# Optimization experiments

Hardware: AMD Instinct MI355X
Metric: run time of the kernel (lower is better)

Reference implementation:

```python
import jax, jax.numpy as jnp
import numpy as np

# ---- layer config (yolov3, layer_no=2) ----
STRIDE = 8
N_CLASSES = 80
IGNORE_TH = 0.7
ANCHORS_PX = np.array([[10,13],[16,30],[33,23],[30,61],[62,45],[59,119],[116,90],[156,198],[373,326]], np.float32)
ALL_ANCHORS = ANCHORS_PX / STRIDE          # [9,2] in grid units
ANCHOR_ID_LO, ANCHOR_ID_HI = 0, 2          # anchor_mask[2] = [0,1,2]
ANCHORS = ALL_ANCHORS[ANCHOR_ID_LO:ANCHOR_ID_HI+1]  # [3,2]
NA = 3
NC = N_CLASSES + 5

B, IN_CH, NG, NBOX = 16, 256, 76, 50


def _safe_log(p):
    # emulate torch BCE's log clamp at -100; eps stops 0*inf -> nan
    return jnp.maximum(jnp.log(jnp.maximum(p, 1e-12)), -100.0)


def _bce_sum(p, t, w=None):
    l = -(t * _safe_log(p) + (1.0 - t) * _safe_log(1.0 - p))
    if w is not None:
        l = l * w
    return l.sum()


def setup_inputs() -> dict:
    key = jax.random.key(0)
    k1, k2, k3, k4, k5 = jax.random.split(key, 5)
    xin = jax.random.normal(k1, (B, IN_CH, NG, NG), jnp.float32)
    cls = jax.random.randint(k2, (B, NBOX, 1), 0, N_CLASSES).astype(jnp.float32)
    cxy = jax.random.uniform(k3, (B, NBOX, 2), jnp.float32, 0.02, 0.98)
    wh = jax.random.uniform(k4, (B, NBOX, 2), jnp.float32, 0.02, 0.40)
    labels = jnp.concatenate([cls, cxy, wh], axis=-1)  # [B,N,5]
    W = jax.random.normal(k5, (NA * NC, IN_CH), jnp.float32) * 0.02  # 1x1 conv
    b = jnp.zeros((NA * NC,), jnp.float32)
    return {"xin": xin, "labels": labels, "W": W, "b": b}


def _yolo_loss(xin, labels, W, b):
    nB, _, nG, _ = xin.shape
    anchors = jnp.asarray(ANCHORS, xin.dtype)          # [3,2]
    all_anchors = jnp.asarray(ALL_ANCHORS, xin.dtype)  # [9,2]

    # 1x1 conv -> [B, A, G, G, C]
    x = jnp.einsum('bchw,oc->bohw', xin, W) + b[None, :, None, None]
    x = x.reshape(nB, NA, NC, nG, nG).transpose(0, 1, 3, 4, 2)

    xy = jax.nn.sigmoid(x[..., :2])
    wh = x[..., 2:4]
    conf_cls = jax.nn.sigmoid(x[..., 4:])  # [B,A,G,G,1+ncls]

    gy, gx = jnp.meshgrid(jnp.arange(nG, dtype=x.dtype), jnp.arange(nG, dtype=x.dtype), indexing='ij')
    pred_boxes = jnp.stack([
        xy[..., 0] + gx,
        xy[..., 1] + gy,
        jnp.exp(wh[..., 0]) * anchors[:, 0][None, :, None, None],
        jnp.exp(wh[..., 1]) * anchors[:, 1][None, :, None, None]], axis=-1)  # [B,A,G,G,4]

    # ---- ground truth ----
    valid = labels.sum(-1) > 0                     # [B,N]
    gt_cls = labels[..., 0].astype(jnp.int32)
    gt = labels[..., 1:] * nG                      # [B,N,4] cx,cy,w,h in grid units
    gt_x, gt_y, gt_w, gt_h = gt[..., 0], gt[..., 1], gt[..., 2], gt[..., 3]
    gi = jnp.floor(gt_x).astype(jnp.int32)
    gj = jnp.floor(gt_y).astype(jnp.int32)

    # best anchor per gt: wh-IoU vs all 9 anchors (centered at origin)
    inter_a = jnp.minimum(gt_w[..., None], all_anchors[:, 0]) * jnp.minimum(gt_h[..., None], all_anchors[:, 1])
    union_a = gt_w[..., None] * gt_h[..., None] + all_anchors[:, 0] * all_anchors[:, 1] - inter_a
    best = jnp.argmax(inter_a / union_a, axis=-1)  # [B,N]
    in_mask = (best >= ANCHOR_ID_LO) & (best <= ANCHOR_ID_HI)
    a = jnp.where(in_mask, best % 3, -1)           # [B,N]

    # all-pairs IoU: pred boxes vs gt boxes (ignore mask)
    pb = pred_boxes.reshape(nB, -1, 4)             # [B,M,4], M = A*G*G
    pa_area = pb[..., 2] * pb[..., 3]
    gt_area = gt_w * gt_h
    tl = jnp.maximum(pb[:, :, None, :2] - pb[:, :, None, 2:] / 2, gt[:, None, :, :2] - gt[:, None, :, 2:] / 2)
    br = jnp.minimum(pb[:, :, None, :2] + pb[:, :, None, 2:] / 2, gt[:, None, :, :2] + gt[:, None, :, 2:] / 2)
    inter = jnp.prod(br - tl, -1) * jnp.all(tl < br, -1)
    iou = inter / (pa_area[:, :, None] + gt_area[:, None, :] - inter)
    iou = jnp.where(valid[:, None, :], iou, 0.0)
    best_iou = iou.max(-1)                         # [B,M]
    has_boxes = valid.any(-1)
    obj_mask = jnp.where(has_boxes[:, None], best_iou <= IGNORE_TH, True).reshape(nB, NA, nG, nG)

    # ---- scatter target assignment ----
    assign = valid & (a >= 0)
    a_safe = jnp.clip(a, 0, NA - 1)
    aw = anchors[a_safe, 0]
    ah = anchors[a_safe, 1]
    tvec = jnp.concatenate([
        (gt_x - jnp.floor(gt_x))[..., None],
        (gt_y - jnp.floor(gt_y))[..., None],
        jnp.log(gt_w / aw + 1e-16)[..., None],
        jnp.log(gt_h / ah + 1e-16)[..., None],
        jnp.ones_like(gt_x)[..., None],
        jax.nn.one_hot(gt_cls, N_CLASSES, dtype=x.dtype)], axis=-1)  # [B,N,NC]
    sval = 2.0 - gt_w * gt_h / (nG * nG)

    bf = jnp.broadcast_to(jnp.arange(nB)[:, None], a.shape).reshape(-1)
    af = jnp.where(assign, a_safe, NA).reshape(-1)  # NA is OOB -> dropped
    jf = gj.reshape(-1)
    if_ = gi.reshape(-1)

    target = jnp.zeros((nB, NA, nG, nG, NC), x.dtype).at[bf, af, jf, if_].set(tvec.reshape(-1, NC), mode='drop')
    scale = jnp.zeros((nB, NA, nG, nG), x.dtype).at[bf, af, jf, if_].set(sval.reshape(-1), mode='drop')
    obj_mask = obj_mask.at[bf, af, jf, if_].set(True, mode='drop')
    noobj = jnp.zeros((nB, NA, nG, nG), bool).at[bf, af, jf, if_].set(True, mode='drop')

    # ---- losses ----
    nm = noobj.astype(x.dtype)[..., None]
    p_obj = conf_cls[..., 0] * obj_mask
    t_obj = target[..., 4] * obj_mask
    p_xy = xy * nm
    t_xy = target[..., :2] * nm
    p_wh = wh * nm
    t_wh = target[..., 2:4] * nm
    p_cls = conf_cls[..., 1:] * nm
    t_cls = target[..., 5:] * nm
    sc = scale[..., None]

    loss_xy = _bce_sum(p_xy, t_xy, sc)
    rs = jnp.sqrt(sc)
    loss_wh = 0.5 * jnp.sum((p_wh * rs - t_wh * rs) ** 2)
    loss_obj = _bce_sum(p_obj, t_obj)
    loss_cls = _bce_sum(p_cls, t_cls)
    loss = loss_xy + loss_wh + loss_obj + loss_cls
    return jnp.stack([loss, loss_xy, loss_wh, loss_obj, loss_cls])


def reference(xin, labels, W, b):
    return _yolo_loss(xin, labels, W, b)
```

## Files before the change

kernel.cpp:

```cpp
#include <hip/hip_runtime.h>
#include <math.h>

#define NB    16
#define NAg   3
#define NCg   85
#define NCLS  80
#define NGg   76
#define NSp   (NGg*NGg)
#define NCELL (NAg*NSp)
#define NBOX  50
#define INCH  256

#define ACC_OFF  0
#define WIN_OFF  32
#define GD_OFF   (WIN_OFF + NB*NCELL*4)
#define GI_OFF   (GD_OFF + NB*NBOX*10*4)
#define PART_OFF (GI_OFF + NB*NBOX*2*4)
#define PART_SZ1 ((size_t)NB*15*NSp*4)
#define NEED4    (PART_OFF + 4*PART_SZ1)
#define NEED1    (PART_OFF + 1*PART_SZ1)
#define ZERO_BYTES GD_OFF

__device__ __constant__ float c_AW[9] = {1.25f,2.0f,4.125f,3.75f,7.75f,7.375f,14.5f,19.5f,46.625f};
__device__ __constant__ float c_AH[9] = {1.625f,3.75f,2.875f,7.625f,5.625f,14.875f,11.25f,24.75f,40.75f};

__device__ __forceinline__ float safe_log(float p) {
    return fmaxf(logf(fmaxf(p, 1e-12f)), -100.0f);
}
__device__ __forceinline__ float sigm(float x) {
    return 1.0f / (1.0f + expf(-x));
}

template<int NSLICE>
__global__ __launch_bounds__(256) void k_gemm_part(
    const float* __restrict__ xin, const float* __restrict__ W,
    float* __restrict__ part)
{
    constexpr int CPS = INCH / NSLICE;
    const int g  = blockIdx.x * 256 + threadIdx.x;
    if (g >= NSp/4) return;
    const int b  = blockIdx.y;
    const int sl = blockIdx.z;
    const int s0 = g * 4;

    float4 acc[15];
#pragma unroll
    for (int f = 0; f < 15; f++) acc[f] = make_float4(0.f,0.f,0.f,0.f);

    const float* xp = xin + ((size_t)b * INCH + sl * CPS) * NSp + s0;
    const float* wp = W + sl * CPS;
#pragma unroll 8
    for (int c = 0; c < CPS; c++) {
        const float4 v = *(const float4*)(xp + (size_t)c * NSp);
#pragma unroll
        for (int f = 0; f < 15; f++) {
            const int row = (f / 5) * NCg + (f % 5);
            const float w = wp[row * INCH + c];
            acc[f].x += w * v.x; acc[f].y += w * v.y;
            acc[f].z += w * v.z; acc[f].w += w * v.w;
        }
    }
#pragma unroll
    for (int f = 0; f < 15; f++)
        *(float4*)&part[(((size_t)sl * NB + b) * 15 + f) * NSp + s0] = acc[f];
}

__global__ void k_labels(const float* __restrict__ labels,
                         float* __restrict__ gdata, int* __restrict__ gint,
                         int* __restrict__ win)
{
    int t = blockIdx.x * blockDim.x + threadIdx.x;
    if (t >= NB * NBOX) return;
    int b = t / NBOX, n = t % NBOX;

    const float* L = labels + (size_t)t * 5;
    float l0 = L[0], l1 = L[1], l2 = L[2], l3 = L[3], l4 = L[4];
    int valid = (l0 + l1 + l2 + l3 + l4) > 0.f;

    float gx = l1 * NGg, gy = l2 * NGg, gw = l3 * NGg, gh = l4 * NGg;

    int best = 0; float brr = -1.f;
#pragma unroll
    for (int k = 0; k < 9; k++) {
        float inter = fminf(gw, c_AW[k]) * fminf(gh, c_AH[k]);
        float uni   = gw*gh + c_AW[k]*c_AH[k] - inter;
        float r     = inter / uni;
        if (r > brr) { brr = r; best = k; }
    }
    int a = (best <= 2) ? best : -1;
    int assign = valid && (a >= 0);
    int a_safe = a < 0 ? 0 : (a > 2 ? 2 : a);

    float* gd = gdata + (size_t)t * 10;
    gd[0] = gx; gd[1] = gy; gd[2] = gw; gd[3] = gh;
    gd[4] = gx - floorf(gx);
    gd[5] = gy - floorf(gy);
    gd[6] = logf(gw / c_AW[a_safe] + 1e-16f);
    gd[7] = logf(gh / c_AH[a_safe] + 1e-16f);
    gd[8] = 2.f - gw * gh / (float)NSp;
    gd[9] = valid ? 1.f : 0.f;

    int gi = (int)floorf(gx), gj = (int)floorf(gy);
    int inb = (gi >= 0) && (gi < NGg) && (gj >= 0) && (gj < NGg);
    int cell = (assign && inb) ? (a * NSp + gj * NGg + gi) : -1;
    gint[t*2 + 0] = cell;
    gint[t*2 + 1] = (int)l0;

    if (cell >= 0) atomicMax(&win[b * NCELL + cell], n + 1);
}

template<int NSLICE>
__global__ __launch_bounds__(256) void k_fuse(
    const float* __restrict__ part, const float* __restrict__ bias,
    const float* __restrict__ gdata, const int* __restrict__ win,
    float* __restrict__ acc)
{
    __shared__ float sb[NBOX][5];
    __shared__ int sHas;
    __shared__ float red[256];

    const int b = blockIdx.y;
    const int tid = threadIdx.x;

    if (tid < NBOX) {
        const float* gd = gdata + ((size_t)b * NBOX + tid) * 10;
        sb[tid][0] = gd[0]; sb[tid][1] = gd[1];
        sb[tid][2] = gd[2]; sb[tid][3] = gd[3];
        sb[tid][4] = gd[9];
    }
    if (tid == 0) sHas = 0;
    __syncthreads();
    if (tid < NBOX && sb[tid][4] > 0.f) atomicOr(&sHas, 1);
    __syncthreads();

    const int cell = blockIdx.x * 256 + tid;
    float l = 0.f;
    if (cell < NCELL) {
        const int a = cell / NSp, s = cell % NSp;
        float x0 = 0.f, x1 = 0.f, x2 = 0.f, x3 = 0.f, x4 = 0.f;
#pragma unroll
        for (int sl = 0; sl < NSLICE; sl++) {
            const float* pp = part + (((size_t)sl * NB + b) * 15 + a * 5) * NSp + s;
            x0 += pp[0*NSp]; x1 += pp[1*NSp]; x2 += pp[2*NSp];
            x3 += pp[3*NSp]; x4 += pp[4*NSp];
        }
        const float gxf = (float)(s % NGg);
        const float gyf = (float)(s / NGg);
        float px = sigm(x0 + bias[a*NCg+0]) + gxf;
        float py = sigm(x1 + bias[a*NCg+1]) + gyf;
        float pw = expf(x2 + bias[a*NCg+2]) * c_AW[a];
        float ph = expf(x3 + bias[a*NCg+3]) * c_AH[a];
        float cf = sigm(x4 + bias[a*NCg+4]);
        float pa = pw * ph;
        float bi = 0.f;
        for (int n = 0; n < NBOX; n++) {
            if (sb[n][4] > 0.f) {
                float gx = sb[n][0], gy = sb[n][1], gw = sb[n][2], gh = sb[n][3];
                float tlx = fmaxf(px - pw*0.5f, gx - gw*0.5f);
                float tly = fmaxf(py - ph*0.5f, gy - gh*0.5f);
                float brx = fminf(px + pw*0.5f, gx + gw*0.5f);
                float bry = fminf(py + ph*0.5f, gy + gh*0.5f);
                float inter = ((tlx < brx) && (tly < bry)) ? (brx-tlx)*(bry-tly) : 0.f;
                float iou = inter / (pa + gw*gh - inter);
                bi = fmaxf(bi, iou);
            }
        }
        bool maskpre  = sHas ? (bi <= 0.7f) : true;
        bool assigned = win[b * NCELL + cell] > 0;
        if (maskpre || assigned) {
            float t = assigned ? 1.f : 0.f;
            l = -(t * safe_log(cf) + (1.f - t) * safe_log(1.f - cf));
        }
    }
    red[tid] = l;
    __syncthreads();
    for (int o = 128; o > 0; o >>= 1) {
        if (tid < o) red[tid] += red[tid + o];
        __syncthreads();
    }
    if (tid == 0) atomicAdd(&acc[2], red[0]);
}

__global__ __launch_bounds__(256) void k_assigned(
    const float* __restrict__ xin, const float* __restrict__ W,
    const float* __restrict__ bias, const float* __restrict__ gdata,
    const int* __restrict__ gint, const int* __restrict__ win,
    float* __restrict__ acc)
{
    const int t = blockIdx.x;
    const int b = t / NBOX, n = t % NBOX;
    const int cell = gint[t*2];
    if (cell < 0) return;
    if (win[b * NCELL + cell] != n + 1) return;

    const int a = cell / NSp, s = cell % NSp;
    const int o0 = a * NCg;
    const int tid = threadIdx.x;

    __shared__ float4 col4[64];
    __shared__ float  xsh[NCg];
    __shared__ float  sacc[3];

    ((float*)col4)[tid] = xin[((size_t)b * INCH + tid) * NSp + s];
    if (tid < 3) sacc[tid] = 0.f;
    __syncthreads();

    const int wid = tid >> 6, lane = tid & 63;
    for (int o = wid; o < NCg; o += 4) {
        const float4 wv = *(const float4*)&W[(size_t)(o0 + o) * INCH + lane * 4];
        const float4 cv = col4[lane];
        float p = wv.x*cv.x + wv.y*cv.y + wv.z*cv.z + wv.w*cv.w;
        for (int off = 32; off; off >>= 1) p += __shfl_down(p, off);
        if (lane == 0) xsh[o] = p + bias[o0 + o];
    }
    __syncthreads();

    if (tid < NCg) {
        const float* gd = gdata + (size_t)t * 10;
        const float sval = gd[8];
        const int gcls = gint[t*2 + 1];
        float val = xsh[tid];
        float term; int slot;
        if (tid < 2) {
            float tgt = gd[4 + tid];
            float p = sigm(val);
            term = -(tgt * safe_log(p) + (1.f - tgt) * safe_log(1.f - p)) * sval;
            slot = 0;
        } else if (tid < 4) {
            float tgt = gd[4 + tid];
            float d = val - tgt;
            term = 0.5f * sval * d * d;
            slot = 1;
        } else if (tid == 4) {
            term = 0.f; slot = 2;
        } else {
            float tgt = ((tid - 5) == gcls) ? 1.f : 0.f;
            float p = sigm(val);
            term = -(tgt * safe_log(p) + (1.f - tgt) * safe_log(1.f - p));
            slot = 2;
        }
        atomicAdd(&sacc[slot], term);
    }
    __syncthreads();
    if (tid == 0) {
        atomicAdd(&acc[0], sacc[0]);
        atomicAdd(&acc[1], sacc[1]);
        atomicAdd(&acc[3], sacc[2]);
    }
}

__global__ void k_final(const float* __restrict__ acc, float* __restrict__ out)
{
    float xy = acc[0], wh = acc[1], ob = acc[2], cl = acc[3];
    out[0] = xy + wh + ob + cl;
    out[1] = xy; out[2] = wh; out[3] = ob; out[4] = cl;
}

extern "C" void kernel_launch(void* const* d_in, const int* in_sizes, int n_in,
                              void* d_out, int out_size, void* d_ws, size_t ws_size,
                              hipStream_t stream)
{
    const float* xin    = (const float*)d_in[0];
    const float* labels = (const float*)d_in[1];
    const float* W      = (const float*)d_in[2];
    const float* bias   = (const float*)d_in[3];

    char* ws = (char*)d_ws;
    float* acc   = (float*)(ws + ACC_OFF);
    int*   win   = (int*)  (ws + WIN_OFF);
    float* gdata = (float*)(ws + GD_OFF);
    int*   gint  = (int*)  (ws + GI_OFF);
    float* part  = (float*)(ws + PART_OFF);
    float* out   = (float*)d_out;

    const bool big = (ws_size >= (size_t)NEED4);

    hipMemsetAsync(ws, 0, ZERO_BYTES, stream);

    k_labels<<<dim3((NB*NBOX + 255)/256), 256, 0, stream>>>(labels, gdata, gint, win);

    const int gx = (NSp/4 + 255) / 256;
    if (big) k_gemm_part<4><<<dim3(gx, NB, 4), 256, 0, stream>>>(xin, W, part);
    else     k_gemm_part<1><<<dim3(gx, NB, 1), 256, 0, stream>>>(xin, W, part);

    const int fx = (NCELL + 255) / 256;
    if (big) k_fuse<4><<<dim3(fx, NB), 256, 0, stream>>>(part, bias, gdata, win, acc);
    else     k_fuse<1><<<dim3(fx, NB), 256, 0, stream>>>(part, bias, gdata, win, acc);

    k_assigned<<<dim3(NB*NBOX), 256, 0, stream>>>(xin, W, bias, gdata, gint, win, acc);
    k_final<<<1, 1, 0, stream>>>(acc, out);
}
```

Measured before the change: 203.1 us.

## Fuse partial GEMM and objectness loss into one kernel, drop winner map

Replaces the sliced partial-GEMM kernel plus the separate fuse kernel with a single kernel in which each thread computes all 15 needed conv outputs for one spatial position across the three anchors, then evaluates IoU and the objectness BCE in registers. A pre-transposed 16-wide weight table is built in the labels kernel. The per-cell winner array, with its large memset and atomics, is replaced by scanning the per-image box list for assignment and duplicate detection. The IoU threshold test is done by multiplication instead of division. This removes the partial-sum buffer round trip and the large zeroing, at the cost of a longer serial channel loop per thread with 64-thread blocks and lower parallelism.

```diff
diff --git a/kernel.cpp b/kernel.cpp
--- a/kernel.cpp
+++ b/kernel.cpp
@@ -7,19 +7,16 @@
 #define NCLS  80
 #define NGg   76
 #define NSp   (NGg*NGg)
-#define NCELL (NAg*NSp)
 #define NBOX  50
 #define INCH  256
 
 #define ACC_OFF  0
-#define WIN_OFF  32
-#define GD_OFF   (WIN_OFF + NB*NCELL*4)
-#define GI_OFF   (GD_OFF + NB*NBOX*10*4)
-#define PART_OFF (GI_OFF + NB*NBOX*2*4)
-#define PART_SZ1 ((size_t)NB*15*NSp*4)
-#define NEED4    (PART_OFF + 4*PART_SZ1)
-#define NEED1    (PART_OFF + 1*PART_SZ1)
-#define ZERO_BYTES GD_OFF
+#define HAS_OFF  32
+#define WT_OFF   128
+#define GB_OFF   (WT_OFF + 16384)
+#define GA_OFF   (GB_OFF + 25600)
+#define GI_OFF   (GA_OFF + 25600)
+#define ZERO_BYTES 96
 
 __device__ __constant__ float c_AW[9] = {1.25f,2.0f,4.125f,3.75f,7.75f,7.375f,14.5f,19.5f,46.625f};
 __device__ __constant__ float c_AH[9] = {1.625f,3.75f,2.875f,7.625f,5.625f,14.875f,11.25f,24.75f,40.75f};
@@ -31,53 +28,25 @@
     return 1.0f / (1.0f + expf(-x));
 }
 
-template<int NSLICE>
-__global__ __launch_bounds__(256) void k_gemm_part(
-    const float* __restrict__ xin, const float* __restrict__ W,
-    float* __restrict__ part)
-{
-    constexpr int CPS = INCH / NSLICE;
-    const int g  = blockIdx.x * 256 + threadIdx.x;
-    if (g >= NSp/4) return;
-    const int b  = blockIdx.y;
-    const int sl = blockIdx.z;
-    const int s0 = g * 4;
-
-    float4 acc[15];
-#pragma unroll
-    for (int f = 0; f < 15; f++) acc[f] = make_float4(0.f,0.f,0.f,0.f);
-
-    const float* xp = xin + ((size_t)b * INCH + sl * CPS) * NSp + s0;
-    const float* wp = W + sl * CPS;
-#pragma unroll 8
-    for (int c = 0; c < CPS; c++) {
-        const float4 v = *(const float4*)(xp + (size_t)c * NSp);
-#pragma unroll
-        for (int f = 0; f < 15; f++) {
-            const int row = (f / 5) * NCg + (f % 5);
-            const float w = wp[row * INCH + c];
-            acc[f].x += w * v.x; acc[f].y += w * v.y;
-            acc[f].z += w * v.z; acc[f].w += w * v.w;
-        }
-    }
-#pragma unroll
-    for (int f = 0; f < 15; f++)
-        *(float4*)&part[(((size_t)sl * NB + b) * 15 + f) * NSp + s0] = acc[f];
-}
-
-__global__ void k_labels(const float* __restrict__ labels,
-                         float* __restrict__ gdata, int* __restrict__ gint,
-                         int* __restrict__ win)
-{
-    int t = blockIdx.x * blockDim.x + threadIdx.x;
+__global__ __launch_bounds__(256) void k_labels(
+    const float* __restrict__ labels, const float* __restrict__ W,
+    float* __restrict__ Wt, float* __restrict__ gbox, float* __restrict__ gaux,
+    int* __restrict__ gint, int* __restrict__ hasAny)
+{
+    const int t = blockIdx.x * 256 + threadIdx.x;
+
+    if (t < INCH * 16) {
+        const int c = t >> 4, f = t & 15;
+        Wt[t] = (f < 15) ? W[((f / 5) * NCg + (f % 5)) * INCH + c] : 0.f;
+    }
     if (t >= NB * NBOX) return;
-    int b = t / NBOX, n = t % NBOX;
+    const int b = t / NBOX;
 
     const float* L = labels + (size_t)t * 5;
-    float l0 = L[0], l1 = L[1], l2 = L[2], l3 = L[3], l4 = L[4];
-    int valid = (l0 + l1 + l2 + l3 + l4) > 0.f;
-
-    float gx = l1 * NGg, gy = l2 * NGg, gw = l3 * NGg, gh = l4 * NGg;
+    const float l0 = L[0], l1 = L[1], l2 = L[2], l3 = L[3], l4 = L[4];
+    const int valid = (l0 + l1 + l2 + l3 + l4) > 0.f;
+
+    const float gx = l1 * NGg, gy = l2 * NGg, gw = l3 * NGg, gh = l4 * NGg;
 
     int best = 0; float brr = -1.f;
 #pragma unroll
@@ -87,111 +56,138 @@
         float r     = inter / uni;
         if (r > brr) { brr = r; best = k; }
     }
-    int a = (best <= 2) ? best : -1;
-    int assign = valid && (a >= 0);
-    int a_safe = a < 0 ? 0 : (a > 2 ? 2 : a);
-
-    float* gd = gdata + (size_t)t * 10;
-    gd[0] = gx; gd[1] = gy; gd[2] = gw; gd[3] = gh;
-    gd[4] = gx - floorf(gx);
-    gd[5] = gy - floorf(gy);
-    gd[6] = logf(gw / c_AW[a_safe] + 1e-16f);
-    gd[7] = logf(gh / c_AH[a_safe] + 1e-16f);
-    gd[8] = 2.f - gw * gh / (float)NSp;
-    gd[9] = valid ? 1.f : 0.f;
-
-    int gi = (int)floorf(gx), gj = (int)floorf(gy);
-    int inb = (gi >= 0) && (gi < NGg) && (gj >= 0) && (gj < NGg);
-    int cell = (assign && inb) ? (a * NSp + gj * NGg + gi) : -1;
+    const int a = (best <= 2) ? best : -1;
+    const int assign = valid && (a >= 0);
+    const int a_safe = a < 0 ? 0 : (a > 2 ? 2 : a);
+
+    const int gi = (int)floorf(gx), gj = (int)floorf(gy);
+    const int inb = (gi >= 0) && (gi < NGg) && (gj >= 0) && (gj < NGg);
+    const int cell = (assign && inb) ? (a * NSp + gj * NGg + gi) : -1;
+
+    float* gb = gbox + (size_t)t * 8;
+    gb[0] = gx - gw * 0.5f;
+    gb[1] = gy - gh * 0.5f;
+    gb[2] = gx + gw * 0.5f;
+    gb[3] = gy + gh * 0.5f;
+    gb[4] = valid ? gw * gh : -1.f;
+    gb[5] = __int_as_float(cell);
+
+    float* ga = gaux + (size_t)t * 8;
+    ga[0] = gx - floorf(gx);
+    ga[1] = gy - floorf(gy);
+    ga[2] = logf(gw / c_AW[a_safe] + 1e-16f);
+    ga[3] = logf(gh / c_AH[a_safe] + 1e-16f);
+    ga[4] = 2.f - gw * gh / (float)NSp;
+
     gint[t*2 + 0] = cell;
     gint[t*2 + 1] = (int)l0;
 
-    if (cell >= 0) atomicMax(&win[b * NCELL + cell], n + 1);
-}
-
-template<int NSLICE>
-__global__ __launch_bounds__(256) void k_fuse(
-    const float* __restrict__ part, const float* __restrict__ bias,
-    const float* __restrict__ gdata, const int* __restrict__ win,
-    float* __restrict__ acc)
-{
-    __shared__ float sb[NBOX][5];
-    __shared__ int sHas;
-    __shared__ float red[256];
-
+    if (valid) atomicOr(&hasAny[b], 1);
+}
+
+__global__ __launch_bounds__(64) void k_main(
+    const float* __restrict__ xin, const float* __restrict__ Wt,
+    const float* __restrict__ bias, const float* __restrict__ gbox,
+    const int* __restrict__ hasAny, float* __restrict__ acc)
+{
     const int b = blockIdx.y;
-    const int tid = threadIdx.x;
-
-    if (tid < NBOX) {
-        const float* gd = gdata + ((size_t)b * NBOX + tid) * 10;
-        sb[tid][0] = gd[0]; sb[tid][1] = gd[1];
-        sb[tid][2] = gd[2]; sb[tid][3] = gd[3];
-        sb[tid][4] = gd[9];
-    }
-    if (tid == 0) sHas = 0;
-    __syncthreads();
-    if (tid < NBOX && sb[tid][4] > 0.f) atomicOr(&sHas, 1);
-    __syncthreads();
-
-    const int cell = blockIdx.x * 256 + tid;
+    const int s = blockIdx.x * 64 + threadIdx.x;
+
     float l = 0.f;
-    if (cell < NCELL) {
-        const int a = cell / NSp, s = cell % NSp;
-        float x0 = 0.f, x1 = 0.f, x2 = 0.f, x3 = 0.f, x4 = 0.f;
-#pragma unroll
-        for (int sl = 0; sl < NSLICE; sl++) {
-            const float* pp = part + (((size_t)sl * NB + b) * 15 + a * 5) * NSp + s;
-            x0 += pp[0*NSp]; x1 += pp[1*NSp]; x2 += pp[2*NSp];
-            x3 += pp[3*NSp]; x4 += pp[4*NSp];
-        }
-        const float gxf = (float)(s % NGg);
-        const float gyf = (float)(s / NGg);
-        float px = sigm(x0 + bias[a*NCg+0]) + gxf;
-        float py = sigm(x1 + bias[a*NCg+1]) + gyf;
-        float pw = expf(x2 + bias[a*NCg+2]) * c_AW[a];
-        float ph = expf(x3 + bias[a*NCg+3]) * c_AH[a];
-        float cf = sigm(x4 + bias[a*NCg+4]);
-        float pa = pw * ph;
-        float bi = 0.f;
-        for (int n = 0; n < NBOX; n++) {
-            if (sb[n][4] > 0.f) {
-                float gx = sb[n][0], gy = sb[n][1], gw = sb[n][2], gh = sb[n][3];
-                float tlx = fmaxf(px - pw*0.5f, gx - gw*0.5f);
-                float tly = fmaxf(py - ph*0.5f, gy - gh*0.5f);
-                float brx = fminf(px + pw*0.5f, gx + gw*0.5f);
-                float bry = fminf(py + ph*0.5f, gy + gh*0.5f);
-                float inter = ((tlx < brx) && (tly < bry)) ? (brx-tlx)*(bry-tly) : 0.f;
-                float iou = inter / (pa + gw*gh - inter);
-                bi = fmaxf(bi, iou);
+    if (s < NSp) {
+        float accv[15];
+#pragma unroll
+        for (int f = 0; f < 15; ++f) accv[f] = 0.f;
+
+        const float* xp = xin + (size_t)b * INCH * NSp + s;
+#pragma unroll 2
+        for (int c0 = 0; c0 < INCH; c0 += 8) {
+            float v[8];
+#pragma unroll
+            for (int k = 0; k < 8; ++k) v[k] = xp[(size_t)(c0 + k) * NSp];
+#pragma unroll
+            for (int k = 0; k < 8; ++k) {
+                const float* wr = Wt + ((c0 + k) << 4);
+#pragma unroll
+                for (int f = 0; f < 15; ++f) accv[f] += wr[f] * v[k];
             }
         }
-        bool maskpre  = sHas ? (bi <= 0.7f) : true;
-        bool assigned = win[b * NCELL + cell] > 0;
-        if (maskpre || assigned) {
-            float t = assigned ? 1.f : 0.f;
-            l = -(t * safe_log(cf) + (1.f - t) * safe_log(1.f - cf));
-        }
-    }
-    red[tid] = l;
-    __syncthreads();
-    for (int o = 128; o > 0; o >>= 1) {
-        if (tid < o) red[tid] += red[tid + o];
-        __syncthreads();
-    }
-    if (tid == 0) atomicAdd(&acc[2], red[0]);
+
+        const int sy = s / NGg;
+        const int sx = s - sy * NGg;
+        const float gxf = (float)sx, gyf = (float)sy;
+
+        float pbx0[3], pby0[3], pbx1[3], pby1[3], pa[3], cf[3];
+#pragma unroll
+        for (int a = 0; a < 3; ++a) {
+            const float px = sigm(accv[a*5+0] + bias[a*NCg+0]) + gxf;
+            const float py = sigm(accv[a*5+1] + bias[a*NCg+1]) + gyf;
+            const float pw = expf(accv[a*5+2] + bias[a*NCg+2]) * c_AW[a];
+            const float ph = expf(accv[a*5+3] + bias[a*NCg+3]) * c_AH[a];
+            cf[a]  = sigm(accv[a*5+4] + bias[a*NCg+4]);
+            pbx0[a] = px - pw * 0.5f;  pby0[a] = py - ph * 0.5f;
+            pbx1[a] = px + pw * 0.5f;  pby1[a] = py + ph * 0.5f;
+            pa[a]   = pw * ph;
+        }
+
+        bool ex0 = false, ex1 = false, ex2 = false;
+        bool as0 = false, as1 = false, as2 = false;
+        const float* gb = gbox + (size_t)b * NBOX * 8;
+        for (int n = 0; n < NBOX; ++n) {
+            const float bx0 = gb[n*8+0], by0 = gb[n*8+1];
+            const float bx1 = gb[n*8+2], by1 = gb[n*8+3];
+            const float gar = gb[n*8+4];
+            const int cell  = __float_as_int(gb[n*8+5]);
+            const int d = cell - s;
+            as0 = as0 || (d == 0);
+            as1 = as1 || (d == NSp);
+            as2 = as2 || (d == 2*NSp);
+            if (gar >= 0.f) {
+#pragma unroll
+                for (int a = 0; a < 3; ++a) {
+                    const float tlx = fmaxf(pbx0[a], bx0);
+                    const float tly = fmaxf(pby0[a], by0);
+                    const float brx = fminf(pbx1[a], bx1);
+                    const float bry = fminf(pby1[a], by1);
+                    const float dx = brx - tlx, dy = bry - tly;
+                    const float inter = (dx > 0.f && dy > 0.f) ? dx * dy : 0.f;
+                    const bool hit = inter > 0.7f * (pa[a] + gar - inter);
+                    if      (a == 0) ex0 = ex0 || hit;
+                    else if (a == 1) ex1 = ex1 || hit;
+                    else             ex2 = ex2 || hit;
+                }
+            }
+        }
+
+        const bool hasB = hasAny[b] != 0;
+#pragma unroll
+        for (int a = 0; a < 3; ++a) {
+            const bool ex = (a == 0) ? ex0 : ((a == 1) ? ex1 : ex2);
+            const bool as = (a == 0) ? as0 : ((a == 1) ? as1 : as2);
+            const bool maskpre = hasB ? (!ex) : true;
+            if (maskpre || as) {
+                const float c = cf[a];
+                l += as ? -safe_log(c) : -safe_log(1.f - c);
+            }
+        }
+    }
+
+#pragma unroll
+    for (int off = 32; off > 0; off >>= 1) l += __shfl_down(l, off);
+    if (threadIdx.x == 0) atomicAdd(&acc[2], l);
 }
 
 __global__ __launch_bounds__(256) void k_assigned(
     const float* __restrict__ xin, const float* __restrict__ W,
-    const float* __restrict__ bias, const float* __restrict__ gdata,
-    const int* __restrict__ gint, const int* __restrict__ win,
-    float* __restrict__ acc)
+    const float* __restrict__ bias, const float* __restrict__ gaux,
+    const int* __restrict__ gint, float* __restrict__ acc)
 {
     const int t = blockIdx.x;
     const int b = t / NBOX, n = t % NBOX;
     const int cell = gint[t*2];
     if (cell < 0) return;
-    if (win[b * NCELL + cell] != n + 1) return;
+    for (int n2 = n + 1; n2 < NBOX; ++n2)
+        if (gint[(b*NBOX + n2)*2] == cell) return;
 
     const int a = cell / NSp, s = cell % NSp;
     const int o0 = a * NCg;
@@ -216,18 +212,18 @@
     __syncthreads();
 
     if (tid < NCg) {
-        const float* gd = gdata + (size_t)t * 10;
-        const float sval = gd[8];
+        const float* ga = gaux + (size_t)t * 8;
+        const float sval = ga[4];
         const int gcls = gint[t*2 + 1];
         float val = xsh[tid];
         float term; int slot;
         if (tid < 2) {
-            float tgt = gd[4 + tid];
+            float tgt = ga[tid];
             float p = sigm(val);
             term = -(tgt * safe_log(p) + (1.f - tgt) * safe_log(1.f - p)) * sval;
             slot = 0;
         } else if (tid < 4) {
-            float tgt = gd[4 + tid];
+            float tgt = ga[tid];
             float d = val - tgt;
             term = 0.5f * sval * d * d;
             slot = 1;
@@ -266,27 +262,21 @@
     const float* bias   = (const float*)d_in[3];
 
     char* ws = (char*)d_ws;
-    float* acc   = (float*)(ws + ACC_OFF);
-    int*   win   = (int*)  (ws + WIN_OFF);
-    float* gdata = (float*)(ws + GD_OFF);
-    int*   gint  = (int*)  (ws + GI_OFF);
-    float* part  = (float*)(ws + PART_OFF);
-    float* out   = (float*)d_out;
-
-    const bool big = (ws_size >= (size_t)NEED4);
+    float* acc    = (float*)(ws + ACC_OFF);
+    int*   hasAny = (int*)  (ws + HAS_OFF);
+    float* Wt     = (float*)(ws + WT_OFF);
+    float* gbox   = (float*)(ws + GB_OFF);
+    float* gaux   = (float*)(ws + GA_OFF);
+    int*   gint   = (int*)  (ws + GI_OFF);
+    float* out    = (float*)d_out;
 
     hipMemsetAsync(ws, 0, ZERO_BYTES, stream);
 
-    k_labels<<<dim3((NB*NBOX + 255)/256), 256, 0, stream>>>(labels, gdata, gint, win);
-
-    const int gx = (NSp/4 + 255) / 256;
-    if (big) k_gemm_part<4><<<dim3(gx, NB, 4), 256, 0, stream>>>(xin, W, part);
-    else     k_gemm_part<1><<<dim3(gx, NB, 1), 256, 0, stream>>>(xin, W, part);
-
-    const int fx = (NCELL + 255) / 256;
-    if (big) k_fuse<4><<<dim3(fx, NB), 256, 0, stream>>>(part, bias, gdata, win, acc);
-    else     k_fuse<1><<<dim3(fx, NB), 256, 0, stream>>>(part, bias, gdata, win, acc);
-
-    k_assigned<<<dim3(NB*NBOX), 256, 0, stream>>>(xin, W, bias, gdata, gint, win, acc);
+    k_labels<<<16, 256, 0, stream>>>(labels, W, Wt, gbox, gaux, gint, hasAny);
+
+    k_main<<<dim3((NSp + 63) / 64, NB), 64, 0, stream>>>(xin, Wt, bias, gbox, hasAny, acc);
+
+    k_assigned<<<dim3(NB * NBOX), 256, 0, stream>>>(xin, W, bias, gaux, gint, acc);
+
     k_final<<<1, 1, 0, stream>>>(acc, out);
 }
```

Measured after the change: 236.1 us. +16.3%, slower.
